# Performance work log

Measured on AMD Instinct MI355X. Metric: run time of the kernel, lower is better.

## Reference

```python
import jax, jax.numpy as jnp
import numpy as np

D_K = 64

def setup_inputs() -> dict:
    key = jax.random.key(0)
    kq, kk, kv, km = jax.random.split(key, 4)
    B, H, S, D = 2, 16, 2048, D_K
    Q = jax.random.normal(kq, (B, H, S, D), dtype=jnp.float32)
    K = jax.random.normal(kk, (B, H, S, D), dtype=jnp.float32)
    V = jax.random.normal(kv, (B, H, S, D), dtype=jnp.float32)
    attn_mask = jax.random.bernoulli(km, 0.9, (B, H, S))  # True = valid
    return {"Q": Q, "K": K, "V": V, "attn_mask": attn_mask}

def reference(Q, K, V, attn_mask):
    # scores: [B, H, S, S]
    scores = jnp.einsum('bhqd,bhkd->bhqk', Q, K) / np.sqrt(D_K).astype(np.float32)
    fill = jnp.float32(1e-9)
    # mask rows (query positions) then columns (key positions), as in original
    scores = jnp.where(attn_mask[..., :, None], scores, fill)
    scores = jnp.where(attn_mask[..., None, :], scores, fill)
    attn = jax.nn.softmax(scores, axis=-1)
    context = jnp.einsum('bhqk,bhkd->bhqd', attn, V)
    return (context, attn)
```

## Files before the change

### kernel.cpp

```cpp
#include <hip/hip_runtime.h>

#define B_DIM 2
#define H_DIM 16
#define S_DIM 2048
#define D_DIM 64

constexpr int KB = 64;
constexpr int NT = S_DIM / KB;
constexpr float CL2E = 0.18033688011112042f;

typedef __attribute__((ext_vector_type(8))) short short8;
typedef __attribute__((ext_vector_type(4))) float f32x4;
typedef __attribute__((ext_vector_type(2))) unsigned uint2v;

__device__ __forceinline__ unsigned pkbf(float lo, float hi) {
  unsigned r;
  asm("v_cvt_pk_bf16_f32 %0, %1, %2" : "=v"(r) : "v"(lo), "v"(hi));
  return r;
}

__device__ __forceinline__ float fexp2(float x) {
  float r;
  asm("v_exp_f32 %0, %1" : "=v"(r) : "v"(x));
  return r;
}

__device__ __forceinline__ void barrier_lds() {
  asm volatile("s_waitcnt lgkmcnt(0)" ::: "memory");
  __builtin_amdgcn_s_barrier();
  asm volatile("" ::: "memory");
}

__global__ __launch_bounds__(512, 2)
void sdpa_kernel(const float* __restrict__ Qp, const float* __restrict__ Kp,
                 const float* __restrict__ Vp, const int* __restrict__ maskp,
                 float* __restrict__ ctx, float* __restrict__ attn)
{
  __shared__ __align__(16) unsigned short sK[2][KB * 64];
  __shared__ __align__(16) unsigned short sV[2][64 * KB];
  __shared__ __align__(16) unsigned short sP[8][16 * 64];

  const int tid  = threadIdx.x;
  const int wave = tid >> 6;
  const int lane = tid & 63;
  const int c = lane & 15;
  const int g = lane >> 4;

  const int bid = (blockIdx.x & 7) * 32 + (blockIdx.x >> 3);
  const int bh = bid >> 3;
  const int qt = bid & 7;
  const int q0x = qt * 256 + wave * 16;
  const int q0y = q0x + 128;
  const size_t bhS = (size_t)bh * S_DIM;

  const int keyk = tid >> 3;
  const int dqk  = (tid & 7) << 3;
  const int kpv  = (tid & 31) << 1;
  const int d4   = (tid >> 5) << 2;

  short8 qfX[2], qfY[2];
  #pragma unroll
  for (int kk = 0; kk < 2; ++kk) {
    const float* sx = Qp + (bhS + (size_t)(q0x + c)) * D_DIM + kk*32 + g*8;
    float4 a = ((const float4*)sx)[0];
    float4 b = ((const float4*)sx)[1];
    union { unsigned u[4]; short8 s; } w;
    w.u[0] = pkbf(a.x, a.y); w.u[1] = pkbf(a.z, a.w);
    w.u[2] = pkbf(b.x, b.y); w.u[3] = pkbf(b.z, b.w);
    qfX[kk] = w.s;
    const float* sy = Qp + (bhS + (size_t)(q0y + c)) * D_DIM + kk*32 + g*8;
    float4 ay = ((const float4*)sy)[0];
    float4 by = ((const float4*)sy)[1];
    w.u[0] = pkbf(ay.x, ay.y); w.u[1] = pkbf(ay.z, ay.w);
    w.u[2] = pkbf(by.x, by.y); w.u[3] = pkbf(by.z, by.w);
    qfY[kk] = w.s;
  }

  const float rvSX = maskp[bhS + q0x + c] ? CL2E : 0.0f;
  const float rvSY = maskp[bhS + q0y + c] ? CL2E : 0.0f;

  float4 kA, kB;
  float4 vA, vB;
  unsigned kmr;

  auto load_k = [&](int kt_) {
    const float* s = Kp + (bhS + (size_t)(kt_ * KB + keyk)) * D_DIM + dqk;
    kA = ((const float4*)s)[0]; kB = ((const float4*)s)[1];
    kmr = maskp[bhS + kt_ * KB + keyk] ? 0xFFFFFFFFu : 0u;
  };
  auto load_v = [&](int kt_) {
    const float* s0 = Vp + (bhS + (size_t)(kt_ * KB + kpv)) * D_DIM + d4;
    vA = *(const float4*)s0;
    vB = *(const float4*)(s0 + D_DIM);
  };
  auto write_k = [&](int buf) {
    union { unsigned u[4]; short8 s; } w;
    w.u[0] = pkbf(kA.x, kA.y) & kmr; w.u[1] = pkbf(kA.z, kA.w) & kmr;
    w.u[2] = pkbf(kB.x, kB.y) & kmr; w.u[3] = pkbf(kB.z, kB.w) & kmr;
    *(short8*)&sK[buf][keyk * 64 + (dqk ^ ((keyk & 7) << 3))] = w.s;
  };
  auto write_v = [&](int buf) {
    float fa[4], fb[4];
    *(float4*)fa = vA; *(float4*)fb = vB;
    #pragma unroll
    for (int e = 0; e < 4; ++e) {
      const int d = d4 + e;
      *(unsigned*)&sV[buf][d * KB + (kpv ^ ((d & 7) << 3))] = pkbf(fa[e], fb[e]);
    }
  };

  unsigned short* const myP = sP[wave];
  const int rh  = lane >> 4;
  const int c16 = lane & 15;
  float* const abx = attn + (bhS + (size_t)q0x) * S_DIM;
  float* const aby = attn + (bhS + (size_t)q0y) * S_DIM;

  auto copyout = [&](float* ab, int kt_) {
    float* const at = ab + kt_*KB;
    #pragma unroll
    for (int j = 0; j < 4; ++j) {
      const int rr = j*4 + rh;
      const int p8 = (c16 >> 1) ^ (rr & 7);
      uint2v u = *(const uint2v*)&myP[rr*64 + p8*8 + (c16 & 1)*4];
      union { unsigned iu; float f; } t0, t1, t2, t3;
      t0.iu = u.x << 16; t1.iu = u.x & 0xFFFF0000u;
      t2.iu = u.y << 16; t3.iu = u.y & 0xFFFF0000u;
      f32x4 o; o[0] = t0.f; o[1] = t1.f; o[2] = t2.f; o[3] = t3.f;
      __builtin_nontemporal_store(o, (f32x4*)(at + (size_t)rr * S_DIM + c16*4));
    }
  };

  auto read_kf = [&](int cur, short8 (&kf)[4][2]) {
    #pragma unroll
    for (int n = 0; n < 4; ++n) {
      const int k2 = n*16 + c;
      const int sw = (c & 7) << 3;
      #pragma unroll
      for (int kk = 0; kk < 2; ++kk)
        kf[n][kk] = *(const short8*)&sK[cur][k2*64 + ((kk*32 + g*8) ^ sw)];
    }
  };

  float lsumX = 0.0f;
  load_k(0);
  for (int kt = 0; kt < NT; ++kt) {
    const int cur = kt & 1;
    write_k(cur);
    if (kt + 1 < NT) load_k(kt + 1);
    else { load_k(0); load_v(0); }
    barrier_lds();

    short8 kf[4][2];
    read_kf(cur, kf);
    f32x4 sacc[4];
    #pragma unroll
    for (int n = 0; n < 4; ++n) sacc[n] = 0.0f;
    __builtin_amdgcn_s_setprio(1);
    #pragma unroll
    for (int n = 0; n < 4; ++n)
      #pragma unroll
      for (int kk = 0; kk < 2; ++kk)
        sacc[n] = __builtin_amdgcn_mfma_f32_16x16x32_bf16(kf[n][kk], qfX[kk], sacc[n], 0, 0, 0);
    __builtin_amdgcn_s_setprio(0);
    #pragma unroll
    for (int n = 0; n < 4; ++n)
      #pragma unroll
      for (int e = 0; e < 4; ++e)
        lsumX += fexp2(sacc[n][e] * rvSX);
  }
  float LmX;
  {
    float v = lsumX;
    v += __shfl_xor(v, 16);
    v += __shfl_xor(v, 32);
    LmX = -__log2f(v);
  }

  f32x4 oaccX[4];
  #pragma unroll
  for (int n = 0; n < 4; ++n) oaccX[n] = 0.0f;
  float lsumY = 0.0f;

  for (int kt = 0; kt < NT; ++kt) {
    const int cur = kt & 1;
    write_k(cur);
    write_v(cur);
    if (kt + 1 < NT) { load_k(kt + 1); load_v(kt + 1); }
    else { load_k(0); load_v(0); }
    barrier_lds();

    short8 kf[4][2];
    read_kf(cur, kf);

    f32x4 saccX[4], saccY[4];
    #pragma unroll
    for (int n = 0; n < 4; ++n) { saccX[n] = 0.0f; saccY[n] = 0.0f; }
    __builtin_amdgcn_s_setprio(1);
    #pragma unroll
    for (int n = 0; n < 4; ++n)
      #pragma unroll
      for (int kk = 0; kk < 2; ++kk) {
        saccX[n] = __builtin_amdgcn_mfma_f32_16x16x32_bf16(kf[n][kk], qfX[kk], saccX[n], 0, 0, 0);
        saccY[n] = __builtin_amdgcn_mfma_f32_16x16x32_bf16(kf[n][kk], qfY[kk], saccY[n], 0, 0, 0);
      }
    __builtin_amdgcn_s_setprio(0);

    #pragma unroll
    for (int n = 0; n < 4; ++n) {
      f32x4 pv;
      #pragma unroll
      for (int e = 0; e < 4; ++e)
        pv[e] = fexp2(__builtin_fmaf(saccX[n][e], rvSX, LmX));
      const int swk = (n*16 + g*4) ^ ((c & 7) << 3);
      uint2v pr; pr.x = pkbf(pv[0], pv[1]); pr.y = pkbf(pv[2], pv[3]);
      *(uint2v*)&myP[c*64 + swk] = pr;
    }

    #pragma unroll
    for (int n = 0; n < 4; ++n)
      #pragma unroll
      for (int e = 0; e < 4; ++e)
        lsumY += fexp2(saccY[n][e] * rvSY);

    short8 pf[2];
    #pragma unroll
    for (int kk = 0; kk < 2; ++kk)
      pf[kk] = *(const short8*)&myP[c*64 + ((kk*32 + g*8) ^ ((c & 7) << 3))];
    __builtin_amdgcn_s_setprio(1);
    #pragma unroll
    for (int n = 0; n < 4; ++n) {
      const int d = n*16 + c;
      const int sw = (d & 7) << 3;
      #pragma unroll
      for (int kk = 0; kk < 2; ++kk) {
        short8 vf = *(const short8*)&sV[cur][d*KB + ((kk*32 + g*8) ^ sw)];
        oaccX[n] = __builtin_amdgcn_mfma_f32_16x16x32_bf16(pf[kk], vf, oaccX[n], 0, 0, 0);
      }
    }
    __builtin_amdgcn_s_setprio(0);

    copyout(abx, kt);
  }

  #pragma unroll
  for (int n = 0; n < 4; ++n)
    #pragma unroll
    for (int e = 0; e < 4; ++e)
      ctx[(bhS + (size_t)(q0x + g*4 + e)) * D_DIM + (size_t)(n*16 + c)] = oaccX[n][e];

  float LmY;
  {
    float v = lsumY;
    v += __shfl_xor(v, 16);
    v += __shfl_xor(v, 32);
    LmY = -__log2f(v);
  }

  f32x4 oaccY[4];
  #pragma unroll
  for (int n = 0; n < 4; ++n) oaccY[n] = 0.0f;

  for (int kt = 0; kt < NT; ++kt) {
    const int cur = kt & 1;
    write_k(cur);
    write_v(cur);
    if (kt + 1 < NT) { load_k(kt + 1); load_v(kt + 1); }
    barrier_lds();

    short8 kf[4][2];
    read_kf(cur, kf);
    f32x4 sacc[4];
    #pragma unroll
    for (int n = 0; n < 4; ++n) sacc[n] = 0.0f;
    __builtin_amdgcn_s_setprio(1);
    #pragma unroll
    for (int n = 0; n < 4; ++n)
      #pragma unroll
      for (int kk = 0; kk < 2; ++kk)
        sacc[n] = __builtin_amdgcn_mfma_f32_16x16x32_bf16(kf[n][kk], qfY[kk], sacc[n], 0, 0, 0);
    __builtin_amdgcn_s_setprio(0);

    #pragma unroll
    for (int n = 0; n < 4; ++n) {
      f32x4 pv;
      #pragma unroll
      for (int e = 0; e < 4; ++e)
        pv[e] = fexp2(__builtin_fmaf(sacc[n][e], rvSY, LmY));
      const int swk = (n*16 + g*4) ^ ((c & 7) << 3);
      uint2v pr; pr.x = pkbf(pv[0], pv[1]); pr.y = pkbf(pv[2], pv[3]);
      *(uint2v*)&myP[c*64 + swk] = pr;
    }

    short8 pf[2];
    #pragma unroll
    for (int kk = 0; kk < 2; ++kk)
      pf[kk] = *(const short8*)&myP[c*64 + ((kk*32 + g*8) ^ ((c & 7) << 3))];
    __builtin_amdgcn_s_setprio(1);
    #pragma unroll
    for (int n = 0; n < 4; ++n) {
      const int d = n*16 + c;
      const int sw = (d & 7) << 3;
      #pragma unroll
      for (int kk = 0; kk < 2; ++kk) {
        short8 vf = *(const short8*)&sV[cur][d*KB + ((kk*32 + g*8) ^ sw)];
        oaccY[n] = __builtin_amdgcn_mfma_f32_16x16x32_bf16(pf[kk], vf, oaccY[n], 0, 0, 0);
      }
    }
    __builtin_amdgcn_s_setprio(0);

    copyout(aby, kt);
  }

  #pragma unroll
  for (int n = 0; n < 4; ++n)
    #pragma unroll
    for (int e = 0; e < 4; ++e)
      ctx[(bhS + (size_t)(q0y + g*4 + e)) * D_DIM + (size_t)(n*16 + c)] = oaccY[n][e];
}

extern "C" void kernel_launch(void* const* d_in, const int* in_sizes, int n_in,
                              void* d_out, int out_size, void* d_ws, size_t ws_size,
                              hipStream_t stream) {
  const float* Q = (const float*)d_in[0];
  const float* K = (const float*)d_in[1];
  const float* V = (const float*)d_in[2];
  const int*   M = (const int*)d_in[3];
  float* ctx  = (float*)d_out;
  float* attn = ctx + (size_t)B_DIM * H_DIM * S_DIM * D_DIM;
  dim3 grid(B_DIM * H_DIM * (S_DIM / 256));
  sdpa_kernel<<<grid, 512, 0, stream>>>(Q, K, V, M, ctx, attn);
}
```

Measured before the change: 145.8 us.

## Halve block size to 4 waves with 128 queries per block

Shrinks each workgroup from 8 to 4 waves, so each block covers 128 query rows instead of 256, and doubles the grid. The K/V staging loaders are remapped so that 256 threads fill the same 64-key tiles, with each thread loading twice as much data. This raises the block count and may improve load balance or occupancy across CUs. The cost is that each K/V tile is now loaded and converted by twice as many blocks, doubling global K/V traffic and conversion work.

```diff
diff --git a/kernel.cpp b/kernel.cpp
--- a/kernel.cpp
+++ b/kernel.cpp
@@ -31,14 +31,14 @@
   asm volatile("" ::: "memory");
 }
 
-__global__ __launch_bounds__(512, 2)
+__global__ __launch_bounds__(256, 2)
 void sdpa_kernel(const float* __restrict__ Qp, const float* __restrict__ Kp,
                  const float* __restrict__ Vp, const int* __restrict__ maskp,
                  float* __restrict__ ctx, float* __restrict__ attn)
 {
   __shared__ __align__(16) unsigned short sK[2][KB * 64];
   __shared__ __align__(16) unsigned short sV[2][64 * KB];
-  __shared__ __align__(16) unsigned short sP[8][16 * 64];
+  __shared__ __align__(16) unsigned short sP[4][16 * 64];
 
   const int tid  = threadIdx.x;
   const int wave = tid >> 6;
@@ -46,17 +46,17 @@
   const int c = lane & 15;
   const int g = lane >> 4;
 
-  const int bid = (blockIdx.x & 7) * 32 + (blockIdx.x >> 3);
-  const int bh = bid >> 3;
-  const int qt = bid & 7;
-  const int q0x = qt * 256 + wave * 16;
-  const int q0y = q0x + 128;
+  const int bid = (blockIdx.x & 7) * 64 + (blockIdx.x >> 3);
+  const int bh = bid >> 4;
+  const int qt = bid & 15;
+  const int q0x = qt * 128 + wave * 16;
+  const int q0y = q0x + 64;
   const size_t bhS = (size_t)bh * S_DIM;
 
-  const int keyk = tid >> 3;
-  const int dqk  = (tid & 7) << 3;
-  const int kpv  = (tid & 31) << 1;
-  const int d4   = (tid >> 5) << 2;
+  const int key = tid >> 2;
+  const int dq  = (tid & 3) << 4;
+  const int kp  = (tid & 31) << 1;
+  const int dq8 = (tid >> 5) << 3;
 
   short8 qfX[2], qfY[2];
   #pragma unroll
@@ -79,33 +79,39 @@
   const float rvSX = maskp[bhS + q0x + c] ? CL2E : 0.0f;
   const float rvSY = maskp[bhS + q0y + c] ? CL2E : 0.0f;
 
-  float4 kA, kB;
-  float4 vA, vB;
+  float4 kr0, kr1, kr2, kr3;
+  float4 vA0, vA1, vB0, vB1;
   unsigned kmr;
 
   auto load_k = [&](int kt_) {
-    const float* s = Kp + (bhS + (size_t)(kt_ * KB + keyk)) * D_DIM + dqk;
-    kA = ((const float4*)s)[0]; kB = ((const float4*)s)[1];
-    kmr = maskp[bhS + kt_ * KB + keyk] ? 0xFFFFFFFFu : 0u;
+    const float* s = Kp + (bhS + (size_t)(kt_ * KB + key)) * D_DIM + dq;
+    kr0 = ((const float4*)s)[0]; kr1 = ((const float4*)s)[1];
+    kr2 = ((const float4*)s)[2]; kr3 = ((const float4*)s)[3];
+    kmr = maskp[bhS + kt_ * KB + key] ? 0xFFFFFFFFu : 0u;
   };
   auto load_v = [&](int kt_) {
-    const float* s0 = Vp + (bhS + (size_t)(kt_ * KB + kpv)) * D_DIM + d4;
-    vA = *(const float4*)s0;
-    vB = *(const float4*)(s0 + D_DIM);
+    const float* s0 = Vp + (bhS + (size_t)(kt_ * KB + kp)) * D_DIM + dq8;
+    vA0 = ((const float4*)s0)[0]; vA1 = ((const float4*)s0)[1];
+    vB0 = ((const float4*)(s0 + D_DIM))[0]; vB1 = ((const float4*)(s0 + D_DIM))[1];
   };
   auto write_k = [&](int buf) {
-    union { unsigned u[4]; short8 s; } w;
-    w.u[0] = pkbf(kA.x, kA.y) & kmr; w.u[1] = pkbf(kA.z, kA.w) & kmr;
-    w.u[2] = pkbf(kB.x, kB.y) & kmr; w.u[3] = pkbf(kB.z, kB.w) & kmr;
-    *(short8*)&sK[buf][keyk * 64 + (dqk ^ ((keyk & 7) << 3))] = w.s;
+    union { unsigned u[4]; short8 s; } w0, w1;
+    w0.u[0] = pkbf(kr0.x, kr0.y) & kmr; w0.u[1] = pkbf(kr0.z, kr0.w) & kmr;
+    w0.u[2] = pkbf(kr1.x, kr1.y) & kmr; w0.u[3] = pkbf(kr1.z, kr1.w) & kmr;
+    w1.u[0] = pkbf(kr2.x, kr2.y) & kmr; w1.u[1] = pkbf(kr2.z, kr2.w) & kmr;
+    w1.u[2] = pkbf(kr3.x, kr3.y) & kmr; w1.u[3] = pkbf(kr3.z, kr3.w) & kmr;
+    const int sw = (key & 7) << 3;
+    *(short8*)&sK[buf][key * 64 + (dq ^ sw)]       = w0.s;
+    *(short8*)&sK[buf][key * 64 + ((dq + 8) ^ sw)] = w1.s;
   };
   auto write_v = [&](int buf) {
-    float fa[4], fb[4];
-    *(float4*)fa = vA; *(float4*)fb = vB;
-    #pragma unroll
-    for (int e = 0; e < 4; ++e) {
-      const int d = d4 + e;
-      *(unsigned*)&sV[buf][d * KB + (kpv ^ ((d & 7) << 3))] = pkbf(fa[e], fb[e]);
+    float fa[8], fb[8];
+    *(float4*)&fa[0] = vA0; *(float4*)&fa[4] = vA1;
+    *(float4*)&fb[0] = vB0; *(float4*)&fb[4] = vB1;
+    #pragma unroll
+    for (int e = 0; e < 8; ++e) {
+      const int d = dq8 + e;
+      *(unsigned*)&sV[buf][d * KB + (kp ^ ((d & 7) << 3))] = pkbf(fa[e], fb[e]);
     }
   };
 
@@ -327,6 +333,6 @@
   const int*   M = (const int*)d_in[3];
   float* ctx  = (float*)d_out;
   float* attn = ctx + (size_t)B_DIM * H_DIM * S_DIM * D_DIM;
-  dim3 grid(B_DIM * H_DIM * (S_DIM / 256));
-  sdpa_kernel<<<grid, 512, 0, stream>>>(Q, K, V, M, ctx, attn);
-}
+  dim3 grid(B_DIM * H_DIM * (S_DIM / 128));
+  sdpa_kernel<<<grid, 256, 0, stream>>>(Q, K, V, M, ctx, attn);
+}
```

New measurement: 155.3 us. +6.5%, slower.
